# Kernel tuning notes

Hardware: AMD Instinct MI355X
Metric: run time of the kernel (lower is better)

Reference implementation:

```python
import jax, jax.numpy as jnp
import numpy as np

N_NODES = 12288
N_FEATURES = 256
KEY_DIM = 128
N_GRAPHS = 192


def setup_inputs() -> dict:
    key = jax.random.key(0)
    k1, k2, k3, k4, k5 = jax.random.split(key, 5)
    node_out = jax.random.normal(k1, (N_NODES, N_FEATURES), dtype=jnp.float32)
    batch = jnp.sort(jax.random.randint(k2, (N_NODES,), 0, N_GRAPHS, dtype=jnp.int64))
    # xavier_uniform: limit = sqrt(6 / (fan_in + fan_out))
    lim_qk = float(np.sqrt(6.0 / (N_FEATURES + KEY_DIM)))
    lim_v = float(np.sqrt(6.0 / (N_FEATURES + N_FEATURES)))
    query_weight = jax.random.uniform(k3, (N_FEATURES, KEY_DIM), jnp.float32, -lim_qk, lim_qk)
    key_weight = jax.random.uniform(k4, (N_FEATURES, KEY_DIM), jnp.float32, -lim_qk, lim_qk)
    value_weight = jax.random.uniform(k5, (N_FEATURES, N_FEATURES), jnp.float32, -lim_v, lim_v)
    return {
        "node_out": node_out,
        "batch": batch,
        "query_weight": query_weight,
        "key_weight": key_weight,
        "value_weight": value_weight,
    }


def reference(node_out, batch, query_weight, key_weight, value_weight):
    n_features = node_out.shape[1]
    Q = node_out @ query_weight            # [N, K]
    K = node_out @ key_weight              # [N, K]
    V = node_out @ value_weight            # [N, F]
    # NOTE: original scales by sqrt(n_features), not sqrt(key_dim)
    scores = (Q @ K.T) / jnp.sqrt(jnp.asarray(n_features, dtype=Q.dtype))  # [N, N]
    mask = batch[:, None] == batch[None, :]  # block-diagonal per-graph mask
    scores = jnp.where(mask, scores, -jnp.inf)
    attn = jax.nn.softmax(scores, axis=-1)   # every row has >=1 valid entry
    context = attn @ V                        # [N, F]
    return jax.ops.segment_sum(context, batch, num_segments=N_GRAPHS)  # [G, F]
```

## Files before the change

kernel.cpp:

```cpp
#include <hip/hip_runtime.h>
#include <hip/hip_bf16.h>

#define N_NODES  12288
#define N_FEAT   256
#define KDIM     128
#define N_GRAPHS 192
#define NMAX     112
#define KSTRIDE_U 68
#define XS_STRIDE_U 132

#define WS_WBUF   1024
#define WS_QB     (WS_WBUF + N_NODES * 4)
#define WS_KB     (WS_QB + N_NODES * 64 * 4)

typedef __bf16 bf16x8 __attribute__((ext_vector_type(8)));
typedef float  f32x4  __attribute__((ext_vector_type(4)));

__device__ __forceinline__ unsigned bf16_rne(float f) {
  unsigned u = __float_as_uint(f);
  return (u + 0x7FFFu + ((u >> 16) & 1u)) >> 16;
}
__device__ __forceinline__ unsigned pack_bf16(float lo, float hi) {
  return bf16_rne(lo) | (bf16_rne(hi) << 16);
}
__device__ __forceinline__ float bf_lo(unsigned u) { return __uint_as_float(u << 16); }
__device__ __forceinline__ float bf_hi(unsigned u) { return __uint_as_float(u & 0xFFFF0000u); }

__device__ __forceinline__ int lb64(const int* __restrict__ batch, int target, int lane) {
  int lo = 0, hi = N_NODES;
  while (hi > lo) {
    int w = hi - lo;
    int step = (w + 63) >> 6;
    int idx = lo + lane * step;
    bool lt = (idx < hi) && (batch[idx] < target);
    unsigned long long b = __ballot(lt);
    int c = __popcll(b);
    if (c == 0) {
      hi = lo;
    } else {
      int nhi = lo + c * step;
      lo = lo + (c - 1) * step + 1;
      hi = (nhi < hi) ? nhi : hi;
    }
  }
  return lo;
}

__global__ __launch_bounds__(512) void attn_fused_k(const float* __restrict__ X,
                                                    const int* __restrict__ batch,
                                                    const float* __restrict__ Wq,
                                                    const float* __restrict__ Wk,
                                                    const float* __restrict__ Wv,
                                                    float* __restrict__ out,
                                                    unsigned* __restrict__ Qb,
                                                    unsigned* __restrict__ Kb,
                                                    float* __restrict__ wbuf) {
  __shared__ unsigned Xs_u[NMAX * XS_STRIDE_U];
  __shared__ unsigned Qs_u[NMAX * KSTRIDE_U];
  __shared__ unsigned Ks_u[NMAX * KSTRIDE_U];
  __shared__ float    w_lds[8][NMAX];
  __shared__ float    red[2][256];
  __shared__ float    Us[256];

  const int tid  = threadIdx.x;
  const int lane = tid & 63;
  const int wv   = tid >> 6;
  const int l15  = lane & 15;
  const int quad = lane >> 4;
  const int g    = blockIdx.x;
  const float BIG = 1e30f;

  union U8 { unsigned u[4]; bf16x8 v; };
  bf16x8 bq0[8], bq1[8];
  {
    const float* wsrc = (wv < 4) ? Wq : Wk;
    const int c0 = (wv & 3) * 32 + l15;
#pragma unroll
    for (int ks = 0; ks < 8; ks++) {
      U8 t0, t1;
#pragma unroll
      for (int p = 0; p < 4; p++) {
        const int k = ks * 32 + quad * 8 + 2 * p;
        const float* r0p = wsrc + (size_t)k * KDIM;
        const float* r1p = wsrc + (size_t)(k + 1) * KDIM;
        t0.u[p] = pack_bf16(r0p[c0], r1p[c0]);
        t1.u[p] = pack_bf16(r0p[c0 + 16], r1p[c0 + 16]);
      }
      bq0[ks] = t0.v;
      bq1[ks] = t1.v;
    }
  }

  const int i0 = lb64(batch, g, lane);
  const int n  = lb64(batch, g + 1, lane) - i0;
  const bool fast = (n <= NMAX);

  unsigned* dst_lds = (wv < 4) ? Qs_u : Ks_u;
  const float scale = (wv < 4) ? 0.0625f : 1.0f;
  const int cb0 = ((2 * wv + 0) & 7) * 16;
  const int cb1 = ((2 * wv + 1) & 7) * 16;

  if (fast) {
    const int ns   = (n + 15) >> 4;
    const int npad = ns * 16;

    for (int idx = tid; idx < npad * 16; idx += 512) {
      int row = idx >> 4, seg = idx & 15;
      unsigned* dst = &Xs_u[row * XS_STRIDE_U + seg * 8];
      if (row < n) {
        const float* xp = &X[(size_t)(i0 + row) * N_FEAT + seg * 16];
        float4 a = *(const float4*)xp;
        float4 b = *(const float4*)(xp + 4);
        float4 c = *(const float4*)(xp + 8);
        float4 d = *(const float4*)(xp + 12);
        *(uint4*)dst       = make_uint4(pack_bf16(a.x, a.y), pack_bf16(a.z, a.w),
                                        pack_bf16(b.x, b.y), pack_bf16(b.z, b.w));
        *(uint4*)(dst + 4) = make_uint4(pack_bf16(c.x, c.y), pack_bf16(c.z, c.w),
                                        pack_bf16(d.x, d.y), pack_bf16(d.z, d.w));
      } else {
        *(uint4*)dst       = make_uint4(0u, 0u, 0u, 0u);
        *(uint4*)(dst + 4) = make_uint4(0u, 0u, 0u, 0u);
      }
    }
    __syncthreads();

    for (int s = 0; s < ns; s++) {
      f32x4 acc0 = (f32x4){0.f, 0.f, 0.f, 0.f};
      f32x4 acc1 = (f32x4){0.f, 0.f, 0.f, 0.f};
#pragma unroll
      for (int ks = 0; ks < 8; ks++) {
        bf16x8 a = *(const bf16x8*)&Xs_u[(s * 16 + l15) * XS_STRIDE_U + ks * 16 + quad * 4];
        acc0 = __builtin_amdgcn_mfma_f32_16x16x32_bf16(a, bq0[ks], acc0, 0, 0, 0);
        acc1 = __builtin_amdgcn_mfma_f32_16x16x32_bf16(a, bq1[ks], acc1, 0, 0, 0);
      }
#pragma unroll
      for (int e = 0; e < 4; e++) {
        const int row = s * 16 + quad * 4 + e;
        unsigned b0 = bf16_rne(acc0[e] * scale);
        unsigned p0 = __shfl_xor((int)b0, 1);
        unsigned b1 = bf16_rne(acc1[e] * scale);
        unsigned p1 = __shfl_xor((int)b1, 1);
        if ((lane & 1) == 0) {
          dst_lds[row * KSTRIDE_U + ((cb0 + l15) >> 1)] = b0 | (p0 << 16);
          dst_lds[row * KSTRIDE_U + ((cb1 + l15) >> 1)] = b1 | (p1 << 16);
        }
      }
    }
    __syncthreads();

    float wl[7];
#pragma unroll
    for (int f = 0; f < 7; f++) wl[f] = 0.f;

    if (wv < ns) {
      const int s = wv;
      const int arow = min(s * 16 + l15, n - 1);
      bf16x8 au[4];
#pragma unroll
      for (int ks = 0; ks < 4; ks++)
        au[ks] = *(const bf16x8*)&Qs_u[arow * KSTRIDE_U + ks * 16 + quad * 4];

      f32x4 acc[7];
#pragma unroll
      for (int f = 0; f < 7; f++) acc[f] = (f32x4){0.f, 0.f, 0.f, 0.f};
#pragma unroll
      for (int f = 0; f < 7; f++) {
#pragma unroll
        for (int ks = 0; ks < 4; ks++) {
          bf16x8 bu = *(const bf16x8*)&Ks_u[(f * 16 + l15) * KSTRIDE_U + ks * 16 + quad * 4];
          acc[f] = __builtin_amdgcn_mfma_f32_16x16x32_bf16(au[ks], bu, acc[f], 0, 0, 0);
        }
      }
#pragma unroll
      for (int f = 0; f < 7; f++)
        if (f * 16 + l15 >= n) {
          acc[f][0] = -BIG; acc[f][1] = -BIG; acc[f][2] = -BIG; acc[f][3] = -BIG;
        }

#pragma unroll
      for (int e = 0; e < 4; e++) {
        float m = -BIG;
#pragma unroll
        for (int f = 0; f < 7; f++) m = fmaxf(m, acc[f][e]);
        m = fmaxf(m, __shfl_xor(m, 1));
        m = fmaxf(m, __shfl_xor(m, 2));
        m = fmaxf(m, __shfl_xor(m, 4));
        m = fmaxf(m, __shfl_xor(m, 8));
        float p[7], l = 0.f;
#pragma unroll
        for (int f = 0; f < 7; f++) { p[f] = __expf(acc[f][e] - m); l += p[f]; }
        l += __shfl_xor(l, 1);
        l += __shfl_xor(l, 2);
        l += __shfl_xor(l, 4);
        l += __shfl_xor(l, 8);
        const int row = s * 16 + quad * 4 + e;
        float inv = (row < n) ? (1.f / l) : 0.f;
#pragma unroll
        for (int f = 0; f < 7; f++) wl[f] = fmaf(p[f], inv, wl[f]);
      }
    }

#pragma unroll
    for (int f = 0; f < 7; f++) {
      wl[f] += __shfl_xor(wl[f], 16);
      wl[f] += __shfl_xor(wl[f], 32);
    }
    if (lane < 16) {
#pragma unroll
      for (int f = 0; f < 7; f++) w_lds[wv][f * 16 + lane] = wl[f];
    }
    __syncthreads();

    if (tid < NMAX) {
      float t = 0.f;
#pragma unroll
      for (int k = 0; k < 8; k++) t += w_lds[k][tid];
      w_lds[0][tid] = t;
    }
    __syncthreads();
  } else {
    for (int idx = tid; idx < n; idx += 512) wbuf[i0 + idx] = 0.f;

    for (int c0 = 0; c0 < n; c0 += NMAX) {
      const int cn  = min(NMAX, n - c0);
      const int cns = (cn + 15) >> 4;
      __syncthreads();
      for (int idx = tid; idx < cns * 16 * 16; idx += 512) {
        int row = idx >> 4, seg = idx & 15;
        unsigned* dst = &Xs_u[row * XS_STRIDE_U + seg * 8];
        if (row < cn) {
          const float* xp = &X[(size_t)(i0 + c0 + row) * N_FEAT + seg * 16];
          float4 a = *(const float4*)xp;
          float4 b = *(const float4*)(xp + 4);
          float4 c = *(const float4*)(xp + 8);
          float4 d = *(const float4*)(xp + 12);
          *(uint4*)dst       = make_uint4(pack_bf16(a.x, a.y), pack_bf16(a.z, a.w),
                                          pack_bf16(b.x, b.y), pack_bf16(b.z, b.w));
          *(uint4*)(dst + 4) = make_uint4(pack_bf16(c.x, c.y), pack_bf16(c.z, c.w),
                                          pack_bf16(d.x, d.y), pack_bf16(d.z, d.w));
        } else {
          *(uint4*)dst       = make_uint4(0u, 0u, 0u, 0u);
          *(uint4*)(dst + 4) = make_uint4(0u, 0u, 0u, 0u);
        }
      }
      __syncthreads();
      unsigned* dstg = (wv < 4) ? Qb : Kb;
      for (int s = 0; s < cns; s++) {
        f32x4 acc0 = (f32x4){0.f, 0.f, 0.f, 0.f};
        f32x4 acc1 = (f32x4){0.f, 0.f, 0.f, 0.f};
#pragma unroll
        for (int ks = 0; ks < 8; ks++) {
          bf16x8 a = *(const bf16x8*)&Xs_u[(s * 16 + l15) * XS_STRIDE_U + ks * 16 + quad * 4];
          acc0 = __builtin_amdgcn_mfma_f32_16x16x32_bf16(a, bq0[ks], acc0, 0, 0, 0);
          acc1 = __builtin_amdgcn_mfma_f32_16x16x32_bf16(a, bq1[ks], acc1, 0, 0, 0);
        }
#pragma unroll
        for (int e = 0; e < 4; e++) {
          const int row = s * 16 + quad * 4 + e;
          unsigned b0 = bf16_rne(acc0[e] * scale);
          unsigned p0 = __shfl_xor((int)b0, 1);
          unsigned b1 = bf16_rne(acc1[e] * scale);
          unsigned p1 = __shfl_xor((int)b1, 1);
          if ((lane & 1) == 0 && row < cn) {
            dstg[(size_t)(i0 + c0 + row) * 64 + ((cb0 + l15) >> 1)] = b0 | (p0 << 16);
            dstg[(size_t)(i0 + c0 + row) * 64 + ((cb1 + l15) >> 1)] = b1 | (p1 << 16);
          }
        }
      }
    }
    __threadfence();
    __syncthreads();

    for (int lr = wv; lr < n; lr += 8) {
      const uint4* qp4 = (const uint4*)&Qb[(size_t)(i0 + lr) * 64];
      float m_run = -BIG, l_run = 0.f;
      for (int jb = 0; jb < n; jb += 64) {
        int j = jb + lane;
        int jc = min(j, n - 1);
        const uint4* kp4 = (const uint4*)&Kb[(size_t)(i0 + jc) * 64];
        float s = 0.f;
        for (int c = 0; c < 16; c++) {
          uint4 Q1 = qp4[c];
          uint4 K1 = kp4[c];
          s = fmaf(bf_lo(Q1.x), bf_lo(K1.x), s); s = fmaf(bf_hi(Q1.x), bf_hi(K1.x), s);
          s = fmaf(bf_lo(Q1.y), bf_lo(K1.y), s); s = fmaf(bf_hi(Q1.y), bf_hi(K1.y), s);
          s = fmaf(bf_lo(Q1.z), bf_lo(K1.z), s); s = fmaf(bf_hi(Q1.z), bf_hi(K1.z), s);
          s = fmaf(bf_lo(Q1.w), bf_lo(K1.w), s); s = fmaf(bf_hi(Q1.w), bf_hi(K1.w), s);
        }
        if (j >= n) s = -BIG;
        float mc = s;
        for (int off = 32; off; off >>= 1) mc = fmaxf(mc, __shfl_xor(mc, off));
        float m_new = fmaxf(m_run, mc);
        float lc = __expf(s - m_new);
        for (int off = 32; off; off >>= 1) lc += __shfl_xor(lc, off);
        l_run = l_run * __expf(m_run - m_new) + lc;
        m_run = m_new;
      }
      float inv = 1.f / l_run;
      for (int jb = 0; jb < n; jb += 64) {
        int j = jb + lane;
        int jc = min(j, n - 1);
        const uint4* kp4 = (const uint4*)&Kb[(size_t)(i0 + jc) * 64];
        float s = 0.f;
        for (int c = 0; c < 16; c++) {
          uint4 Q1 = qp4[c];
          uint4 K1 = kp4[c];
          s = fmaf(bf_lo(Q1.x), bf_lo(K1.x), s); s = fmaf(bf_hi(Q1.x), bf_hi(K1.x), s);
          s = fmaf(bf_lo(Q1.y), bf_lo(K1.y), s); s = fmaf(bf_hi(Q1.y), bf_hi(K1.y), s);
          s = fmaf(bf_lo(Q1.z), bf_lo(K1.z), s); s = fmaf(bf_hi(Q1.z), bf_hi(K1.z), s);
          s = fmaf(bf_lo(Q1.w), bf_lo(K1.w), s); s = fmaf(bf_hi(Q1.w), bf_hi(K1.w), s);
        }
        if (j < n) atomicAdd(&wbuf[i0 + j], __expf(s - m_run) * inv);
      }
    }
    __threadfence();
    __syncthreads();
  }

  const int f  = tid & 255;
  const int jp = tid >> 8;
  float u0 = 0.f, u1 = 0.f, u2 = 0.f, u3 = 0.f;
  if (fast) {
    int j = jp;
    for (; j + 6 < n; j += 8) {
      u0 = fmaf(w_lds[0][j],     X[(size_t)(i0 + j) * N_FEAT + f], u0);
      u1 = fmaf(w_lds[0][j + 2], X[(size_t)(i0 + j + 2) * N_FEAT + f], u1);
      u2 = fmaf(w_lds[0][j + 4], X[(size_t)(i0 + j + 4) * N_FEAT + f], u2);
      u3 = fmaf(w_lds[0][j + 6], X[(size_t)(i0 + j + 6) * N_FEAT + f], u3);
    }
    for (; j < n; j += 2)
      u0 = fmaf(w_lds[0][j], X[(size_t)(i0 + j) * N_FEAT + f], u0);
  } else {
    for (int j = jp; j < n; j += 2) {
      float wj = atomicAdd(&wbuf[i0 + j], 0.f);
      u0 = fmaf(wj, X[(size_t)(i0 + j) * N_FEAT + f], u0);
    }
  }
  red[jp][f] = (u0 + u1) + (u2 + u3);
  __syncthreads();
  if (jp == 0) Us[f] = red[0][f] + red[1][f];
  __syncthreads();

  const int k0 = jp * 128;
  const float* wp = Wv + (size_t)k0 * N_FEAT + f;
  const float* us = &Us[k0];
  float a0 = 0.f, a1 = 0.f, a2 = 0.f, a3 = 0.f;
#pragma unroll 8
  for (int k = 0; k < 128; k += 4) {
    a0 = fmaf(us[k],     wp[(size_t)k * N_FEAT], a0);
    a1 = fmaf(us[k + 1], wp[(size_t)(k + 1) * N_FEAT], a1);
    a2 = fmaf(us[k + 2], wp[(size_t)(k + 2) * N_FEAT], a2);
    a3 = fmaf(us[k + 3], wp[(size_t)(k + 3) * N_FEAT], a3);
  }
  __syncthreads();
  red[jp][f] = (a0 + a1) + (a2 + a3);
  __syncthreads();
  if (jp == 0) out[g * N_FEAT + f] = red[0][f] + red[1][f];
}

extern "C" void kernel_launch(void* const* d_in, const int* in_sizes, int n_in,
                              void* d_out, int out_size, void* d_ws, size_t ws_size,
                              hipStream_t stream) {
  const float* X     = (const float*)d_in[0];
  const int*   batch = (const int*)d_in[1];
  const float* Wq    = (const float*)d_in[2];
  const float* Wk    = (const float*)d_in[3];
  const float* Wv    = (const float*)d_in[4];
  float* out = (float*)d_out;

  char* ws = (char*)d_ws;
  float*    wbuf = (float*)(ws + WS_WBUF);
  unsigned* Qb   = (unsigned*)(ws + WS_QB);
  unsigned* Kb   = (unsigned*)(ws + WS_KB);

  attn_fused_k<<<N_GRAPHS, 512, 0, stream>>>(X, batch, Wq, Wk, Wv, out, Qb, Kb, wbuf);
}
```

Measured before the change: 82.19 us.

## Double block size to 1024 threads and split per-graph work across 16 waves

The block grows from 8 to 16 waves. Each wave now computes one 16-column slice of Q or K instead of two, and the V-side reduction and the Wv matvec are split four ways instead of two. The two boundary searches run in separate waves and are shared through LDS rather than being repeated by every wave. The goal is more latency hiding and more parallelism per graph, since the grid is only 192 blocks. In exchange it costs more register pressure per thread under the 1024 launch bound, and the score stage still uses only the first few waves.

```diff
diff --git a/kernel.cpp b/kernel.cpp
--- a/kernel.cpp
+++ b/kernel.cpp
@@ -46,21 +46,22 @@
   return lo;
 }
 
-__global__ __launch_bounds__(512) void attn_fused_k(const float* __restrict__ X,
-                                                    const int* __restrict__ batch,
-                                                    const float* __restrict__ Wq,
-                                                    const float* __restrict__ Wk,
-                                                    const float* __restrict__ Wv,
-                                                    float* __restrict__ out,
-                                                    unsigned* __restrict__ Qb,
-                                                    unsigned* __restrict__ Kb,
-                                                    float* __restrict__ wbuf) {
+__global__ __launch_bounds__(1024) void attn_fused_k(const float* __restrict__ X,
+                                                     const int* __restrict__ batch,
+                                                     const float* __restrict__ Wq,
+                                                     const float* __restrict__ Wk,
+                                                     const float* __restrict__ Wv,
+                                                     float* __restrict__ out,
+                                                     unsigned* __restrict__ Qb,
+                                                     unsigned* __restrict__ Kb,
+                                                     float* __restrict__ wbuf) {
   __shared__ unsigned Xs_u[NMAX * XS_STRIDE_U];
   __shared__ unsigned Qs_u[NMAX * KSTRIDE_U];
   __shared__ unsigned Ks_u[NMAX * KSTRIDE_U];
-  __shared__ float    w_lds[8][NMAX];
-  __shared__ float    red[2][256];
+  __shared__ float    w_lds[16][NMAX];
+  __shared__ float    red[4][256];
   __shared__ float    Us[256];
+  __shared__ int      seg[2];
 
   const int tid  = threadIdx.x;
   const int lane = tid & 63;
@@ -71,44 +72,48 @@
   const float BIG = 1e30f;
 
   union U8 { unsigned u[4]; bf16x8 v; };
-  bf16x8 bq0[8], bq1[8];
+  bf16x8 bq[8];
   {
-    const float* wsrc = (wv < 4) ? Wq : Wk;
-    const int c0 = (wv & 3) * 32 + l15;
+    const float* wsrc = (wv < 8) ? Wq : Wk;
+    const int cw = (wv & 7) * 16 + l15;
 #pragma unroll
     for (int ks = 0; ks < 8; ks++) {
-      U8 t0, t1;
+      U8 t;
 #pragma unroll
       for (int p = 0; p < 4; p++) {
         const int k = ks * 32 + quad * 8 + 2 * p;
-        const float* r0p = wsrc + (size_t)k * KDIM;
-        const float* r1p = wsrc + (size_t)(k + 1) * KDIM;
-        t0.u[p] = pack_bf16(r0p[c0], r1p[c0]);
-        t1.u[p] = pack_bf16(r0p[c0 + 16], r1p[c0 + 16]);
-      }
-      bq0[ks] = t0.v;
-      bq1[ks] = t1.v;
-    }
-  }
-
-  const int i0 = lb64(batch, g, lane);
-  const int n  = lb64(batch, g + 1, lane) - i0;
+        t.u[p] = pack_bf16(wsrc[(size_t)k * KDIM + cw],
+                           wsrc[(size_t)(k + 1) * KDIM + cw]);
+      }
+      bq[ks] = t.v;
+    }
+  }
+
+  if (wv == 0) {
+    int r = lb64(batch, g, lane);
+    if (lane == 0) seg[0] = r;
+  } else if (wv == 1) {
+    int r = lb64(batch, g + 1, lane);
+    if (lane == 0) seg[1] = r;
+  }
+  __syncthreads();
+  const int i0 = seg[0];
+  const int n  = seg[1] - i0;
   const bool fast = (n <= NMAX);
 
-  unsigned* dst_lds = (wv < 4) ? Qs_u : Ks_u;
-  const float scale = (wv < 4) ? 0.0625f : 1.0f;
-  const int cb0 = ((2 * wv + 0) & 7) * 16;
-  const int cb1 = ((2 * wv + 1) & 7) * 16;
+  unsigned* dst_lds = (wv < 8) ? Qs_u : Ks_u;
+  const float scale = (wv < 8) ? 0.0625f : 1.0f;
+  const int cb = (wv & 7) * 16;
 
   if (fast) {
     const int ns   = (n + 15) >> 4;
     const int npad = ns * 16;
 
-    for (int idx = tid; idx < npad * 16; idx += 512) {
-      int row = idx >> 4, seg = idx & 15;
-      unsigned* dst = &Xs_u[row * XS_STRIDE_U + seg * 8];
+    for (int idx = tid; idx < npad * 16; idx += 1024) {
+      int row = idx >> 4, sg = idx & 15;
+      unsigned* dst = &Xs_u[row * XS_STRIDE_U + sg * 8];
       if (row < n) {
-        const float* xp = &X[(size_t)(i0 + row) * N_FEAT + seg * 16];
+        const float* xp = &X[(size_t)(i0 + row) * N_FEAT + sg * 16];
         float4 a = *(const float4*)xp;
         float4 b = *(const float4*)(xp + 4);
         float4 c = *(const float4*)(xp + 8);
@@ -125,25 +130,19 @@
     __syncthreads();
 
     for (int s = 0; s < ns; s++) {
-      f32x4 acc0 = (f32x4){0.f, 0.f, 0.f, 0.f};
-      f32x4 acc1 = (f32x4){0.f, 0.f, 0.f, 0.f};
+      f32x4 acc = (f32x4){0.f, 0.f, 0.f, 0.f};
 #pragma unroll
       for (int ks = 0; ks < 8; ks++) {
         bf16x8 a = *(const bf16x8*)&Xs_u[(s * 16 + l15) * XS_STRIDE_U + ks * 16 + quad * 4];
-        acc0 = __builtin_amdgcn_mfma_f32_16x16x32_bf16(a, bq0[ks], acc0, 0, 0, 0);
-        acc1 = __builtin_amdgcn_mfma_f32_16x16x32_bf16(a, bq1[ks], acc1, 0, 0, 0);
+        acc = __builtin_amdgcn_mfma_f32_16x16x32_bf16(a, bq[ks], acc, 0, 0, 0);
       }
 #pragma unroll
       for (int e = 0; e < 4; e++) {
         const int row = s * 16 + quad * 4 + e;
-        unsigned b0 = bf16_rne(acc0[e] * scale);
+        unsigned b0 = bf16_rne(acc[e] * scale);
         unsigned p0 = __shfl_xor((int)b0, 1);
-        unsigned b1 = bf16_rne(acc1[e] * scale);
-        unsigned p1 = __shfl_xor((int)b1, 1);
-        if ((lane & 1) == 0) {
-          dst_lds[row * KSTRIDE_U + ((cb0 + l15) >> 1)] = b0 | (p0 << 16);
-          dst_lds[row * KSTRIDE_U + ((cb1 + l15) >> 1)] = b1 | (p1 << 16);
-        }
+        if ((lane & 1) == 0)
+          dst_lds[row * KSTRIDE_U + ((cb + l15) >> 1)] = b0 | (p0 << 16);
       }
     }
     __syncthreads();
@@ -214,22 +213,23 @@
     if (tid < NMAX) {
       float t = 0.f;
 #pragma unroll
-      for (int k = 0; k < 8; k++) t += w_lds[k][tid];
+      for (int k = 0; k < 16; k++) t += w_lds[k][tid];
       w_lds[0][tid] = t;
     }
     __syncthreads();
   } else {
-    for (int idx = tid; idx < n; idx += 512) wbuf[i0 + idx] = 0.f;
-
-    for (int c0 = 0; c0 < n; c0 += NMAX) {
-      const int cn  = min(NMAX, n - c0);
+    for (int idx = tid; idx < n; idx += 1024) wbuf[i0 + idx] = 0.f;
+
+    unsigned* dstg = (wv < 8) ? Qb : Kb;
+    for (int ch = 0; ch < n; ch += NMAX) {
+      const int cn  = min(NMAX, n - ch);
       const int cns = (cn + 15) >> 4;
       __syncthreads();
-      for (int idx = tid; idx < cns * 16 * 16; idx += 512) {
-        int row = idx >> 4, seg = idx & 15;
-        unsigned* dst = &Xs_u[row * XS_STRIDE_U + seg * 8];
+      for (int idx = tid; idx < cns * 16 * 16; idx += 1024) {
+        int row = idx >> 4, sg = idx & 15;
+        unsigned* dst = &Xs_u[row * XS_STRIDE_U + sg * 8];
         if (row < cn) {
-          const float* xp = &X[(size_t)(i0 + c0 + row) * N_FEAT + seg * 16];
+          const float* xp = &X[(size_t)(i0 + ch + row) * N_FEAT + sg * 16];
           float4 a = *(const float4*)xp;
           float4 b = *(const float4*)(xp + 4);
           float4 c = *(const float4*)(xp + 8);
@@ -244,34 +244,27 @@
         }
       }
       __syncthreads();
-      unsigned* dstg = (wv < 4) ? Qb : Kb;
       for (int s = 0; s < cns; s++) {
-        f32x4 acc0 = (f32x4){0.f, 0.f, 0.f, 0.f};
-        f32x4 acc1 = (f32x4){0.f, 0.f, 0.f, 0.f};
+        f32x4 acc = (f32x4){0.f, 0.f, 0.f, 0.f};
 #pragma unroll
         for (int ks = 0; ks < 8; ks++) {
           bf16x8 a = *(const bf16x8*)&Xs_u[(s * 16 + l15) * XS_STRIDE_U + ks * 16 + quad * 4];
-          acc0 = __builtin_amdgcn_mfma_f32_16x16x32_bf16(a, bq0[ks], acc0, 0, 0, 0);
-          acc1 = __builtin_amdgcn_mfma_f32_16x16x32_bf16(a, bq1[ks], acc1, 0, 0, 0);
+          acc = __builtin_amdgcn_mfma_f32_16x16x32_bf16(a, bq[ks], acc, 0, 0, 0);
         }
 #pragma unroll
         for (int e = 0; e < 4; e++) {
           const int row = s * 16 + quad * 4 + e;
-          unsigned b0 = bf16_rne(acc0[e] * scale);
+          unsigned b0 = bf16_rne(acc[e] * scale);
           unsigned p0 = __shfl_xor((int)b0, 1);
-          unsigned b1 = bf16_rne(acc1[e] * scale);
-          unsigned p1 = __shfl_xor((int)b1, 1);
-          if ((lane & 1) == 0 && row < cn) {
-            dstg[(size_t)(i0 + c0 + row) * 64 + ((cb0 + l15) >> 1)] = b0 | (p0 << 16);
-            dstg[(size_t)(i0 + c0 + row) * 64 + ((cb1 + l15) >> 1)] = b1 | (p1 << 16);
-          }
+          if ((lane & 1) == 0 && row < cn)
+            dstg[(size_t)(i0 + ch + row) * 64 + ((cb + l15) >> 1)] = b0 | (p0 << 16);
         }
       }
     }
     __threadfence();
     __syncthreads();
 
-    for (int lr = wv; lr < n; lr += 8) {
+    for (int lr = wv; lr < n; lr += 16) {
       const uint4* qp4 = (const uint4*)&Qb[(size_t)(i0 + lr) * 64];
       float m_run = -BIG, l_run = 0.f;
       for (int jb = 0; jb < n; jb += 64) {
@@ -319,34 +312,32 @@
 
   const int f  = tid & 255;
   const int jp = tid >> 8;
-  float u0 = 0.f, u1 = 0.f, u2 = 0.f, u3 = 0.f;
+  float u0 = 0.f, u1 = 0.f;
   if (fast) {
     int j = jp;
-    for (; j + 6 < n; j += 8) {
+    for (; j + 4 < n; j += 8) {
       u0 = fmaf(w_lds[0][j],     X[(size_t)(i0 + j) * N_FEAT + f], u0);
-      u1 = fmaf(w_lds[0][j + 2], X[(size_t)(i0 + j + 2) * N_FEAT + f], u1);
-      u2 = fmaf(w_lds[0][j + 4], X[(size_t)(i0 + j + 4) * N_FEAT + f], u2);
-      u3 = fmaf(w_lds[0][j + 6], X[(size_t)(i0 + j + 6) * N_FEAT + f], u3);
-    }
-    for (; j < n; j += 2)
+      u1 = fmaf(w_lds[0][j + 4], X[(size_t)(i0 + j + 4) * N_FEAT + f], u1);
+    }
+    for (; j < n; j += 4)
       u0 = fmaf(w_lds[0][j], X[(size_t)(i0 + j) * N_FEAT + f], u0);
   } else {
-    for (int j = jp; j < n; j += 2) {
+    for (int j = jp; j < n; j += 4) {
       float wj = atomicAdd(&wbuf[i0 + j], 0.f);
       u0 = fmaf(wj, X[(size_t)(i0 + j) * N_FEAT + f], u0);
     }
   }
-  red[jp][f] = (u0 + u1) + (u2 + u3);
-  __syncthreads();
-  if (jp == 0) Us[f] = red[0][f] + red[1][f];
-  __syncthreads();
-
-  const int k0 = jp * 128;
+  red[jp][f] = u0 + u1;
+  __syncthreads();
+  if (jp == 0) Us[f] = (red[0][f] + red[1][f]) + (red[2][f] + red[3][f]);
+  __syncthreads();
+
+  const int k0 = jp * 64;
   const float* wp = Wv + (size_t)k0 * N_FEAT + f;
   const float* us = &Us[k0];
   float a0 = 0.f, a1 = 0.f, a2 = 0.f, a3 = 0.f;
-#pragma unroll 8
-  for (int k = 0; k < 128; k += 4) {
+#pragma unroll 4
+  for (int k = 0; k < 64; k += 4) {
     a0 = fmaf(us[k],     wp[(size_t)k * N_FEAT], a0);
     a1 = fmaf(us[k + 1], wp[(size_t)(k + 1) * N_FEAT], a1);
     a2 = fmaf(us[k + 2], wp[(size_t)(k + 2) * N_FEAT], a2);
@@ -355,7 +346,8 @@
   __syncthreads();
   red[jp][f] = (a0 + a1) + (a2 + a3);
   __syncthreads();
-  if (jp == 0) out[g * N_FEAT + f] = red[0][f] + red[1][f];
+  if (jp == 0)
+    out[g * N_FEAT + f] = (red[0][f] + red[1][f]) + (red[2][f] + red[3][f]);
 }
 
 extern "C" void kernel_launch(void* const* d_in, const int* in_sizes, int n_in,
@@ -373,5 +365,5 @@
   unsigned* Qb   = (unsigned*)(ws + WS_QB);
   unsigned* Kb   = (unsigned*)(ws + WS_KB);
 
-  attn_fused_k<<<N_GRAPHS, 512, 0, stream>>>(X, batch, Wq, Wk, Wv, out, Qb, Kb, wbuf);
-}
+  attn_fused_k<<<N_GRAPHS, 1024, 0, stream>>>(X, batch, Wq, Wk, Wv, out, Qb, Kb, wbuf);
+}
```

Measured after the change: 82.16 us. Within noise of the previous version (-0.0%).
